# Kernel optimization log

Hardware: AMD Instinct MI355X
Metric: run time of the kernel (lower is better)

The kernel has to match this reference:

```python
import jax, jax.numpy as jnp
import numpy as np

B, T, C = 4, 2048, 2048
N_HEAD = 16
HEAD_DIM = C // N_HEAD
ROPE_BASE = 10000.0


def setup_inputs() -> dict:
    key = jax.random.key(0)
    k1, k2, k3 = jax.random.split(key, 3)
    x = jax.random.normal(k1, (B, T, C), dtype=jnp.float32)
    Wqkv = jax.random.normal(k2, (C, 3 * C), dtype=jnp.float32) * 0.02
    bqkv = jnp.zeros((3 * C,), dtype=jnp.float32)
    Wproj = jax.random.normal(k3, (C, C), dtype=jnp.float32) * 0.02
    bproj = jnp.zeros((C,), dtype=jnp.float32)
    return {"x": x, "Wqkv": Wqkv, "bqkv": bqkv, "Wproj": Wproj, "bproj": bproj}


def _rope_cos_sin(seq_len, head_dim, dtype):
    inv_freq = 1.0 / (ROPE_BASE ** (jnp.arange(0, head_dim, 2, dtype=jnp.float32) / head_dim))
    t = jnp.arange(seq_len, dtype=jnp.float32)
    freqs = jnp.einsum("i,j->ij", t, inv_freq)          # [T, D/2]
    emb = jnp.concatenate([freqs, freqs], axis=-1)       # [T, D]
    return jnp.cos(emb).astype(dtype), jnp.sin(emb).astype(dtype)


def _rotate_half(x):
    half = x.shape[-1] // 2
    x1, x2 = x[..., :half], x[..., half:]
    return jnp.concatenate([-x2, x1], axis=-1)


def reference(x, Wqkv, bqkv, Wproj, bproj):
    b, t, c = x.shape
    qkv = x @ Wqkv + bqkv                                # [B, T, 3C]
    q, k, v = jnp.split(qkv, 3, axis=-1)
    # [B, T, C] -> [B, H, T, D]
    def to_heads(u):
        return u.reshape(b, t, N_HEAD, HEAD_DIM).transpose(0, 2, 1, 3)
    q, k, v = to_heads(q), to_heads(k), to_heads(v)
    cos, sin = _rope_cos_sin(t, HEAD_DIM, x.dtype)       # [T, D]
    cos = cos[None, None]                                # [1, 1, T, D]
    sin = sin[None, None]
    q = q * cos + _rotate_half(q) * sin
    k = k * cos + _rotate_half(k) * sin
    scale = 1.0 / np.sqrt(HEAD_DIM).astype(np.float32)
    scores = jnp.einsum("bhqd,bhkd->bhqk", q, k) * scale  # [B, H, T, T]
    causal = jnp.tril(jnp.ones((t, t), dtype=bool))
    scores = jnp.where(causal[None, None], scores, jnp.finfo(scores.dtype).min)
    att = jax.nn.softmax(scores, axis=-1)
    y = jnp.einsum("bhqk,bhkd->bhqd", att, v)             # [B, H, T, D]
    y = y.transpose(0, 2, 1, 3).reshape(b, t, c)
    return y @ Wproj + bproj
```

## Files before the change

kernel.cpp:

```cpp
#include <hip/hip_runtime.h>
#include <hip/hip_bf16.h>
#include <stdint.h>
#include <math.h>

#define NB 4
#define NT 2048
#define NC 2048
#define NH 16
#define HD 128
#define BT (NB*NT)

typedef __attribute__((ext_vector_type(8))) short s16x8;
typedef __attribute__((ext_vector_type(4))) short s16x4;
typedef __attribute__((ext_vector_type(4))) float f32x4;

typedef __attribute__((address_space(1))) void as1_void;
typedef __attribute__((address_space(3))) void as3_void;

static __device__ __forceinline__ unsigned short f2bf(float f) {
  union { float f; uint32_t u; } v; v.f = f;
  return (unsigned short)((v.u + 0x7fffu + ((v.u >> 16) & 1u)) >> 16);
}
static __device__ __forceinline__ float bf2f(unsigned short u) {
  union { uint32_t u; float f; } v; v.u = ((uint32_t)u) << 16;
  return v.f;
}
static __device__ __forceinline__ void async16(unsigned short* lds, const unsigned short* g) {
  __builtin_amdgcn_global_load_lds((as1_void*)g, (as3_void*)lds, 16, 0, 0);
}
static __device__ __forceinline__ uint32_t lds_off(void* p) {
  return (uint32_t)(size_t)(as3_void*)p;
}

__global__ void k_convert_bf16(const float* __restrict__ in, unsigned short* __restrict__ out, int n8) {
  int i = blockIdx.x * blockDim.x + threadIdx.x;
  if (i >= n8) return;
  const float4* p = (const float4*)in + (size_t)i * 2;
  float4 a = p[0], b = p[1];
  union { unsigned short s[8]; uint4 u; } o;
  o.s[0] = f2bf(a.x); o.s[1] = f2bf(a.y); o.s[2] = f2bf(a.z); o.s[3] = f2bf(a.w);
  o.s[4] = f2bf(b.x); o.s[5] = f2bf(b.y); o.s[6] = f2bf(b.z); o.s[7] = f2bf(b.w);
  ((uint4*)out)[i] = o.u;
}

__global__ void k_transpose_bf16(const float* __restrict__ W, unsigned short* __restrict__ WT, int K, int N) {
  __shared__ unsigned short tile[64][65];
  const int k0 = blockIdx.y * 64, n0 = blockIdx.x * 64;
  const int t = threadIdx.x;
  const int jj = t & 63, base_i = t >> 6;
  #pragma unroll
  for (int p = 0; p < 16; ++p) {
    int i = p * 4 + base_i;
    tile[i][jj] = f2bf(W[(size_t)(k0 + i) * N + n0 + jj]);
  }
  __syncthreads();
  #pragma unroll
  for (int p = 0; p < 16; ++p) {
    int j = p * 4 + base_i;
    WT[(size_t)(n0 + j) * K + k0 + jj] = tile[jj][j];
  }
}

__global__ void k_rope(unsigned short* __restrict__ Q, unsigned short* __restrict__ Kb) {
  int idx = blockIdx.x * 256 + threadIdx.x;
  int d = idx & 63;
  int tpos = (idx >> 6) & (NT - 1);
  int bh = idx >> 17;
  size_t o = ((size_t)bh * NT + tpos) * HD + d;
  float invf = exp2f(-(float)d * 0.2076205059304602f);
  float ang = (float)tpos * invf;
  float s, c;
  sincosf(ang, &s, &c);
  float q1 = bf2f(Q[o]),  q2 = bf2f(Q[o + 64]);
  float k1 = bf2f(Kb[o]), k2 = bf2f(Kb[o + 64]);
  const float qs = 0.08838834764831845f * 1.4426950408889634f;
  Q[o]       = f2bf((q1 * c - q2 * s) * qs);
  Q[o + 64]  = f2bf((q2 * c + q1 * s) * qs);
  Kb[o]      = f2bf(k1 * c - k2 * s);
  Kb[o + 64] = f2bf(k2 * c + k1 * s);
}

template<int MODE>
__global__ __launch_bounds__(256, 2)
void k_gemm_bt(const unsigned short* __restrict__ A,
               const unsigned short* __restrict__ Bt,
               const float* __restrict__ bias,
               float* __restrict__ OutF,
               unsigned short* __restrict__ Qd,
               unsigned short* __restrict__ Kd,
               unsigned short* __restrict__ Vd,
               int M, int N, int K)
{
  __shared__ __align__(16) unsigned short Al[128 * 64];
  __shared__ __align__(16) unsigned short Bl[128 * 64];
  const int t = threadIdx.x;
  const int l = t & 63;
  const int wv = t >> 6;
  const int wm = wv >> 1, wn = wv & 1;
  const int bm = blockIdx.y * 128, bn = blockIdx.x * 128;
  const int lr = l & 15, lg = l >> 4;

  f32x4 acc[4][4];
  #pragma unroll
  for (int i = 0; i < 4; ++i)
    #pragma unroll
    for (int j = 0; j < 4; ++j)
      acc[i][j] = f32x4{0.f, 0.f, 0.f, 0.f};

  for (int k0 = 0; k0 < K; k0 += 64) {
    #pragma unroll
    for (int i = 0; i < 4; ++i) {
      const int Cc = i * 256 + t;
      const int row = Cc >> 3;
      const int kc = (Cc & 7) ^ (row & 7);
      async16(&Al[(i * 256 + (t & 192)) * 8], &A[(size_t)(bm + row) * K + k0 + kc * 8]);
      async16(&Bl[(i * 256 + (t & 192)) * 8], &Bt[(size_t)(bn + row) * K + k0 + kc * 8]);
    }
    __syncthreads();
    #pragma unroll
    for (int kk = 0; kk < 2; ++kk) {
      s16x8 af[4], bfr[4];
      #pragma unroll
      for (int mb = 0; mb < 4; ++mb) {
        const int row = wm * 64 + mb * 16 + lr;
        const int ch = (kk * 4 + lg) ^ (row & 7);
        af[mb] = *(const s16x8*)&Al[row * 64 + ch * 8];
      }
      #pragma unroll
      for (int nb = 0; nb < 4; ++nb) {
        const int row = wn * 64 + nb * 16 + lr;
        const int ch = (kk * 4 + lg) ^ (row & 7);
        bfr[nb] = *(const s16x8*)&Bl[row * 64 + ch * 8];
      }
      __builtin_amdgcn_s_setprio(1);
      #pragma unroll
      for (int mb = 0; mb < 4; ++mb)
        #pragma unroll
        for (int nb = 0; nb < 4; ++nb)
          acc[mb][nb] = __builtin_amdgcn_mfma_f32_16x16x32_bf16(af[mb], bfr[nb], acc[mb][nb], 0, 0, 0);
      __builtin_amdgcn_s_setprio(0);
    }
    __syncthreads();
  }

  #pragma unroll
  for (int mb = 0; mb < 4; ++mb) {
    #pragma unroll
    for (int nb = 0; nb < 4; ++nb) {
      const int col = bn + wn * 64 + nb * 16 + lr;
      const float bv = bias[col];
      #pragma unroll
      for (int r = 0; r < 4; ++r) {
        const int row = bm + wm * 64 + mb * 16 + lg * 4 + r;
        const float v = acc[mb][nb][r] + bv;
        if (MODE == 1) {
          OutF[(size_t)row * N + col] = v;
        } else {
          const int which = col >> 11;
          const int cc = col & 2047;
          const int h = cc >> 7, d = cc & 127;
          const int b = row >> 11, tp = row & 2047;
          unsigned short* dst = (which == 0) ? Qd : (which == 1 ? Kd : Vd);
          dst[(((size_t)(b * NH + h)) * NT + tp) * HD + d] = f2bf(v);
        }
      }
    }
  }
}

__global__ __launch_bounds__(256, 2)
void k_attn(const unsigned short* __restrict__ Q,
            const unsigned short* __restrict__ Kg,
            const unsigned short* __restrict__ Vg,
            unsigned short* __restrict__ Yatt)
{
  __shared__ __align__(16) unsigned short Kl[64 * 128];
  __shared__ __align__(16) unsigned short Vl[64 * 128];
  const int bh = blockIdx.x;
  const int pair = blockIdx.y;
  const int b = bh >> 4, h = bh & 15;
  const int t = threadIdx.x, l = t & 63, wv = t >> 6;
  const int lr = l & 15, lg = l >> 4;
  const size_t hoff = (size_t)bh * NT * HD;
  const unsigned short* Qh = Q + hoff;
  const unsigned short* Kh = Kg + hoff;
  const unsigned short* Vh = Vg + hoff;
  const uint32_t vbase = lds_off(Vl);

  #pragma unroll 1
  for (int rep = 0; rep < 2; ++rep) {
    const int qb = rep ? (31 - pair) : pair;
    const int q0w = qb * 64 + wv * 16;
    const int qrow = q0w + lr;

    s16x8 qf[4];
    #pragma unroll
    for (int m = 0; m < 4; ++m)
      qf[m] = *(const s16x8*)(Qh + (size_t)qrow * HD + m * 32 + lg * 8);

    f32x4 yt[8];
    #pragma unroll
    for (int n = 0; n < 8; ++n) yt[n] = f32x4{0.f, 0.f, 0.f, 0.f};
    float mrun = -1e30f, lrun = 0.f;

    const int nkv = qb + 1;
    for (int kv = 0; kv < nkv; ++kv) {
      const int kv0 = kv * 64;
      #pragma unroll
      for (int i = 0; i < 4; ++i) {
        const int Cc = i * 256 + t;
        {
          const int krow = Cc >> 4;
          const int kc = (Cc & 15) ^ (krow & 7);
          async16(&Kl[(i * 256 + (t & 192)) * 8], &Kh[(size_t)(kv0 + krow) * HD + kc * 8]);
        }
        {
          const int S = Cc >> 3, c8 = Cc & 7;
          const int kq = S >> 3, dq = S & 7;
          const int vk = kq * 4 + (c8 >> 1), vd = dq * 16 + (c8 & 1) * 8;
          async16(&Vl[(i * 256 + (t & 192)) * 8], &Vh[(size_t)(kv0 + vk) * HD + vd]);
        }
      }
      __syncthreads();

      f32x4 st[4];
      __builtin_amdgcn_s_setprio(1);
      #pragma unroll
      for (int kt = 0; kt < 4; ++kt) {
        f32x4 a = f32x4{0.f, 0.f, 0.f, 0.f};
        const int krow = kt * 16 + lr;
        #pragma unroll
        for (int m = 0; m < 4; ++m) {
          const int ch = (m * 4 + lg) ^ (krow & 7);
          s16x8 kf = *(const s16x8*)&Kl[krow * 128 + ch * 8];
          a = __builtin_amdgcn_mfma_f32_16x16x32_bf16(kf, qf[m], a, 0, 0, 0);
        }
        st[kt] = a;
      }
      __builtin_amdgcn_s_setprio(0);

      if (kv0 + 63 > q0w) {
        #pragma unroll
        for (int kt = 0; kt < 4; ++kt)
          #pragma unroll
          for (int r = 0; r < 4; ++r) {
            const int key = kv0 + kt * 16 + lg * 4 + r;
            if (key > qrow) st[kt][r] = -3.0e38f;
          }
      }

      float tm = -3.0e38f;
      #pragma unroll
      for (int kt = 0; kt < 4; ++kt)
        #pragma unroll
        for (int r = 0; r < 4; ++r) tm = fmaxf(tm, st[kt][r]);
      tm = fmaxf(tm, __shfl_xor(tm, 16));
      tm = fmaxf(tm, __shfl_xor(tm, 32));
      const float mnew = fmaxf(mrun, tm);
      const float fsc = exp2f(mrun - mnew);
      mrun = mnew;
      lrun *= fsc;
      #pragma unroll
      for (int n = 0; n < 8; ++n)
        #pragma unroll
        for (int r = 0; r < 4; ++r) yt[n][r] *= fsc;

      unsigned short pb[16];
      float psum = 0.f;
      #pragma unroll
      for (int kt = 0; kt < 4; ++kt)
        #pragma unroll
        for (int r = 0; r < 4; ++r) {
          const float p = exp2f(st[kt][r] - mnew);
          psum += p;
          pb[kt * 4 + r] = f2bf(p);
        }
      lrun += psum;

      s16x8 pf[2];
      #pragma unroll
      for (int gk = 0; gk < 2; ++gk)
        #pragma unroll
        for (int j = 0; j < 8; ++j)
          pf[gk][j] = (short)pb[(gk * 2 + (j >> 2)) * 4 + (j & 3)];

      #pragma unroll
      for (int gk = 0; gk < 2; ++gk) {
        s16x4 va[8], vb2[8];
        #pragma unroll
        for (int n = 0; n < 8; ++n) {
          const uint32_t a0 = vbase + ((uint32_t)((gk * 8 + lg) * 8 + n)) * 128 + (uint32_t)lr * 8;
          asm volatile("ds_read_b64_tr_b16 %0, %1" : "=v"(va[n])  : "v"(a0));
          asm volatile("ds_read_b64_tr_b16 %0, %1" : "=v"(vb2[n]) : "v"(a0 + 4096));
        }
        asm volatile("s_waitcnt lgkmcnt(0)" ::: "memory");
        __builtin_amdgcn_sched_barrier(0);
        __builtin_amdgcn_s_setprio(1);
        #pragma unroll
        for (int n = 0; n < 8; ++n) {
          s16x8 vf;
          vf[0] = va[n][0];  vf[1] = va[n][1];  vf[2] = va[n][2];  vf[3] = va[n][3];
          vf[4] = vb2[n][0]; vf[5] = vb2[n][1]; vf[6] = vb2[n][2]; vf[7] = vb2[n][3];
          yt[n] = __builtin_amdgcn_mfma_f32_16x16x32_bf16(vf, pf[gk], yt[n], 0, 0, 0);
        }
        __builtin_amdgcn_s_setprio(0);
      }
      __syncthreads();
    }

    lrun += __shfl_xor(lrun, 16);
    lrun += __shfl_xor(lrun, 32);
    const float inv = 1.f / lrun;
    unsigned short* yrow = Yatt + (size_t)(b * NT + q0w + lr) * NC + h * HD;
    #pragma unroll
    for (int n = 0; n < 8; ++n)
      #pragma unroll
      for (int r = 0; r < 4; ++r)
        yrow[n * 16 + lg * 4 + r] = f2bf(yt[n][r] * inv);
  }
}

extern "C" void kernel_launch(void* const* d_in, const int* in_sizes, int n_in,
                              void* d_out, int out_size, void* d_ws, size_t ws_size,
                              hipStream_t stream) {
  (void)in_sizes; (void)n_in; (void)out_size; (void)ws_size;
  const float* x     = (const float*)d_in[0];
  const float* Wqkv  = (const float*)d_in[1];
  const float* bqkv  = (const float*)d_in[2];
  const float* Wproj = (const float*)d_in[3];
  const float* bproj = (const float*)d_in[4];
  float* out = (float*)d_out;
  char* ws = (char*)d_ws;

  unsigned short* xb     = (unsigned short*)(ws);
  unsigned short* WqkvT  = (unsigned short*)(ws + 33554432);
  unsigned short* WprojT = (unsigned short*)(ws + 58720256);
  unsigned short* Qb     = (unsigned short*)(ws + 67108864);
  unsigned short* Kb     = (unsigned short*)(ws + 100663296);
  unsigned short* Vb     = (unsigned short*)(ws + 134217728);
  unsigned short* att    = xb;

  k_convert_bf16<<<dim3(8192), dim3(256), 0, stream>>>(x, xb, BT * NC / 8);
  k_transpose_bf16<<<dim3(96, 32), dim3(256), 0, stream>>>(Wqkv, WqkvT, NC, 3 * NC);
  k_transpose_bf16<<<dim3(32, 32), dim3(256), 0, stream>>>(Wproj, WprojT, NC, NC);
  k_gemm_bt<0><<<dim3(48, 64), dim3(256), 0, stream>>>(xb, WqkvT, bqkv, nullptr, Qb, Kb, Vb, BT, 3 * NC, NC);
  k_rope<<<dim3(32768), dim3(256), 0, stream>>>(Qb, Kb);
  k_attn<<<dim3(64, 16), dim3(256), 0, stream>>>(Qb, Kb, Vb, att);
  k_gemm_bt<1><<<dim3(16, 64), dim3(256), 0, stream>>>(att, WprojT, bproj, out, nullptr, nullptr, nullptr, BT, NC, NC);
}
```

Before: 476.2 us.

## Use 256x256 tiles with double-buffered async LDS staging in GEMMs

New measurement: 470.8 us. About the same (-1.1%).

```diff
diff --git a/kernel.cpp b/kernel.cpp
--- a/kernel.cpp
+++ b/kernel.cpp
@@ -81,8 +81,8 @@
 }
 
 template<int MODE>
-__global__ __launch_bounds__(256, 2)
-void k_gemm_bt(const unsigned short* __restrict__ A,
+__global__ __launch_bounds__(512, 2)
+void k_gemm256(const unsigned short* __restrict__ A,
                const unsigned short* __restrict__ Bt,
                const float* __restrict__ bias,
                float* __restrict__ OutF,
@@ -91,68 +91,87 @@
                unsigned short* __restrict__ Vd,
                int M, int N, int K)
 {
-  __shared__ __align__(16) unsigned short Al[128 * 64];
-  __shared__ __align__(16) unsigned short Bl[128 * 64];
+  __shared__ __align__(16) unsigned short Al[2][256 * 64];
+  __shared__ __align__(16) unsigned short Bl[2][256 * 64];
   const int t = threadIdx.x;
   const int l = t & 63;
   const int wv = t >> 6;
-  const int wm = wv >> 1, wn = wv & 1;
-  const int bm = blockIdx.y * 128, bn = blockIdx.x * 128;
+  const int wm = wv >> 2, wn = wv & 3;
+  const int bm = blockIdx.y * 256, bn = blockIdx.x * 256;
   const int lr = l & 15, lg = l >> 4;
 
-  f32x4 acc[4][4];
+  f32x4 acc[8][4];
   #pragma unroll
-  for (int i = 0; i < 4; ++i)
+  for (int i = 0; i < 8; ++i)
     #pragma unroll
     for (int j = 0; j < 4; ++j)
       acc[i][j] = f32x4{0.f, 0.f, 0.f, 0.f};
 
-  for (int k0 = 0; k0 < K; k0 += 64) {
+  const int ubase = (t & 448) * 8;
+
+  auto stage = [&](int buf, int k0) {
     #pragma unroll
     for (int i = 0; i < 4; ++i) {
-      const int Cc = i * 256 + t;
+      const int Cc = i * 512 + t;
       const int row = Cc >> 3;
       const int kc = (Cc & 7) ^ (row & 7);
-      async16(&Al[(i * 256 + (t & 192)) * 8], &A[(size_t)(bm + row) * K + k0 + kc * 8]);
-      async16(&Bl[(i * 256 + (t & 192)) * 8], &Bt[(size_t)(bn + row) * K + k0 + kc * 8]);
+      async16(&Al[buf][(i * 512) * 8 + ubase], &A[(size_t)(bm + row) * K + k0 + kc * 8]);
+      async16(&Bl[buf][(i * 512) * 8 + ubase], &Bt[(size_t)(bn + row) * K + k0 + kc * 8]);
     }
-    __syncthreads();
+  };
+
+  auto compute = [&](int buf) {
     #pragma unroll
     for (int kk = 0; kk < 2; ++kk) {
-      s16x8 af[4], bfr[4];
-      #pragma unroll
-      for (int mb = 0; mb < 4; ++mb) {
-        const int row = wm * 64 + mb * 16 + lr;
+      s16x8 af[8], bfr[4];
+      #pragma unroll
+      for (int mi = 0; mi < 8; ++mi) {
+        const int row = wm * 128 + mi * 16 + lr;
         const int ch = (kk * 4 + lg) ^ (row & 7);
-        af[mb] = *(const s16x8*)&Al[row * 64 + ch * 8];
-      }
-      #pragma unroll
-      for (int nb = 0; nb < 4; ++nb) {
-        const int row = wn * 64 + nb * 16 + lr;
+        af[mi] = *(const s16x8*)&Al[buf][row * 64 + ch * 8];
+      }
+      #pragma unroll
+      for (int ni = 0; ni < 4; ++ni) {
+        const int row = wn * 64 + ni * 16 + lr;
         const int ch = (kk * 4 + lg) ^ (row & 7);
-        bfr[nb] = *(const s16x8*)&Bl[row * 64 + ch * 8];
+        bfr[ni] = *(const s16x8*)&Bl[buf][row * 64 + ch * 8];
       }
       __builtin_amdgcn_s_setprio(1);
       #pragma unroll
-      for (int mb = 0; mb < 4; ++mb)
-        #pragma unroll
-        for (int nb = 0; nb < 4; ++nb)
-          acc[mb][nb] = __builtin_amdgcn_mfma_f32_16x16x32_bf16(af[mb], bfr[nb], acc[mb][nb], 0, 0, 0);
+      for (int mi = 0; mi < 8; ++mi)
+        #pragma unroll
+        for (int ni = 0; ni < 4; ++ni)
+          acc[mi][ni] = __builtin_amdgcn_mfma_f32_16x16x32_bf16(af[mi], bfr[ni], acc[mi][ni], 0, 0, 0);
       __builtin_amdgcn_s_setprio(0);
     }
-    __syncthreads();
-  }
+  };
+
+  stage(0, 0);
+  const int nkt = K >> 6;
+  int cur = 0;
+  #pragma unroll 1
+  for (int tt = 0; tt < nkt - 1; ++tt) {
+    stage(cur ^ 1, (tt + 1) << 6);
+    asm volatile("s_waitcnt vmcnt(8)" ::: "memory");
+    __builtin_amdgcn_s_barrier();
+    compute(cur);
+    __builtin_amdgcn_s_barrier();
+    cur ^= 1;
+  }
+  asm volatile("s_waitcnt vmcnt(0)" ::: "memory");
+  __builtin_amdgcn_s_barrier();
+  compute(cur);
 
   #pragma unroll
-  for (int mb = 0; mb < 4; ++mb) {
-    #pragma unroll
-    for (int nb = 0; nb < 4; ++nb) {
-      const int col = bn + wn * 64 + nb * 16 + lr;
+  for (int mi = 0; mi < 8; ++mi) {
+    #pragma unroll
+    for (int ni = 0; ni < 4; ++ni) {
+      const int col = bn + wn * 64 + ni * 16 + lr;
       const float bv = bias[col];
       #pragma unroll
       for (int r = 0; r < 4; ++r) {
-        const int row = bm + wm * 64 + mb * 16 + lg * 4 + r;
-        const float v = acc[mb][nb][r] + bv;
+        const int row = bm + wm * 128 + mi * 16 + lg * 4 + r;
+        const float v = acc[mi][ni][r] + bv;
         if (MODE == 1) {
           OutF[(size_t)row * N + col] = v;
         } else {
@@ -343,8 +362,8 @@
   k_convert_bf16<<<dim3(8192), dim3(256), 0, stream>>>(x, xb, BT * NC / 8);
   k_transpose_bf16<<<dim3(96, 32), dim3(256), 0, stream>>>(Wqkv, WqkvT, NC, 3 * NC);
   k_transpose_bf16<<<dim3(32, 32), dim3(256), 0, stream>>>(Wproj, WprojT, NC, NC);
-  k_gemm_bt<0><<<dim3(48, 64), dim3(256), 0, stream>>>(xb, WqkvT, bqkv, nullptr, Qb, Kb, Vb, BT, 3 * NC, NC);
+  k_gemm256<0><<<dim3(24, 32), dim3(512), 0, stream>>>(xb, WqkvT, bqkv, nullptr, Qb, Kb, Vb, BT, 3 * NC, NC);
   k_rope<<<dim3(32768), dim3(256), 0, stream>>>(Qb, Kb);
   k_attn<<<dim3(64, 16), dim3(256), 0, stream>>>(Qb, Kb, Vb, att);
-  k_gemm_bt<1><<<dim3(16, 64), dim3(256), 0, stream>>>(att, WprojT, bproj, out, nullptr, nullptr, nullptr, BT, NC, NC);
-}
+  k_gemm256<1><<<dim3(8, 32), dim3(512), 0, stream>>>(att, WprojT, bproj, out, nullptr, nullptr, nullptr, BT, NC, NC);
+}
```
